# Optimization experiments

Measured on AMD Instinct MI355X. Metric: run time of the kernel, lower is better.

Reference implementation:

```python
import jax, jax.numpy as jnp
import numpy as np

H = 8
DH = 64  # attention_head_size
HID = 512
NEG = -90000000000.0

def _lin(x, w, b):
    return x @ w + b

def _tfs(x):  # [N, HID] -> [H, N, DH]
    n = x.shape[0]
    return x.reshape(n, H, DH).transpose(1, 0, 2)

def _cross(q, ck, v, cv, mask, dw, db):
    # q: [H,N,DH], ck/cv: [H,M,DH], v: [H,N,DH], mask: [N,M]
    s = jnp.einsum('hnd,hmd->hnm', q, ck)
    s = s * mask[None, :, :] / jnp.sqrt(jnp.asarray(DH, s.dtype))
    s = jnp.where(s == 0.0, NEG, s)  # faithful zero->-inf hack
    p = jax.nn.softmax(s, axis=-1)
    ctx = v + jnp.einsum('hnm,hmd->hnd', p, cv)  # residual add of raw value
    n = ctx.shape[1]
    ctx = ctx.transpose(1, 0, 2).reshape(n, H * DH)
    return _lin(ctx, dw, db)

def setup_inputs() -> dict:
    key = jax.random.key(0)
    ks = jax.random.split(key, 24)
    N1, N2, D1 = 4096, 4096, 300
    d = {}
    d['h_head'] = jax.random.normal(ks[0], (N1, D1), jnp.float32)
    d['h_tail'] = jax.random.normal(ks[1], (N2, HID), jnp.float32)
    d['batch_head'] = jnp.sort(jax.random.randint(ks[2], (N1,), 0, 64))
    d['batch_tail'] = jnp.sort(jax.random.randint(ks[3], (N2,), 0, 64))
    def w(k, i, o):
        return jax.random.normal(k, (i, o), jnp.float32) / np.sqrt(i)
    d['map_w'] = w(ks[4], D1, HID); d['map_b'] = jnp.zeros((HID,), jnp.float32)
    names = ['q1', 'k1', 'v1', 'q2', 'k2', 'v2', 'd1', 'd2']
    for i, nm in enumerate(names):
        d[nm + '_w'] = w(ks[5 + i], HID, HID)
        d[nm + '_b'] = jnp.zeros((HID,), jnp.float32)
    return d

def reference(h_head, h_tail, batch_head, batch_tail,
              map_w, map_b,
              q1_w, q1_b, k1_w, k1_b, v1_w, v1_b,
              q2_w, q2_b, k2_w, k2_b, v2_w, v2_b,
              d1_w, d1_b, d2_w, d2_b):
    hh = _lin(h_head, map_w, map_b)  # n_dim1 != n_dim2 -> map
    q_h = _tfs(_lin(hh, q1_w, q1_b))
    k_h = _tfs(_lin(hh, k1_w, k1_b))
    v_h = _tfs(_lin(hh, v1_w, v1_b))
    q_t = _tfs(_lin(h_tail, q2_w, q2_b))
    k_t = _tfs(_lin(h_tail, k2_w, k2_b))
    v_t = _tfs(_lin(h_tail, v2_w, v2_b))
    mask = (batch_head[:, None] == batch_tail[None, :]).astype(jnp.float32)
    out_head = _cross(q_h, k_t, v_h, v_t, mask, d1_w, d1_b)
    out_tail = _cross(q_t, k_h, v_t, v_h, mask.T, d2_w, d2_b)
    return (out_head, out_tail)
```

## Files before the change

### kernel.cpp

```cpp
#include <hip/hip_runtime.h>
#include <hip/hip_bf16.h>
#include <math.h>


typedef __bf16 bf16x8 __attribute__((ext_vector_type(8)));
typedef float  f32x4  __attribute__((ext_vector_type(4)));

#define HID 512
#define NTOK 4096

#define AS1(p) ((const __attribute__((address_space(1))) void*)(p))
#define AS3(p) ((__attribute__((address_space(3))) void*)(p))

__global__ __launch_bounds__(256) void prep_inputs(
    const float* __restrict__ h_head, const float* __restrict__ h_tail,
    const int* __restrict__ bh, const int* __restrict__ bt,
    __bf16* __restrict__ hh_bf, __bf16* __restrict__ ht_bf,
    int* __restrict__ ranges)
{
    const int q = blockIdx.x, z = blockIdx.z, tid = threadIdx.x;

    if (z == 0) {
        if (q == 0 && tid < 128) {
            int b = tid & 63;
            const int* arr = (tid < 64) ? bh : bt;
            int base = (tid < 64) ? 0 : 128;
            int lo = 0, hi = NTOK;
            while (lo < hi) { int mid = (lo + hi) >> 1; if (arr[mid] < b) lo = mid + 1; else hi = mid; }
            int start = lo;
            lo = 0; hi = NTOK;
            while (lo < hi) { int mid = (lo + hi) >> 1; if (arr[mid] <= b) lo = mid + 1; else hi = mid; }
            ranges[base + b] = start;
            ranges[base + 64 + b] = lo;
        }
        for (int idx = tid; idx < 8 * 40; idx += 256) {
            int r   = q * 8 + idx / 40;
            int col = (idx % 40) * 8;
            bf16x8 v;
            if (col + 8 <= 300) {
                float4 f0 = *(const float4*)&h_head[(size_t)r * 300 + col];
                float4 f1 = *(const float4*)&h_head[(size_t)r * 300 + col + 4];
                v[0]=(__bf16)f0.x; v[1]=(__bf16)f0.y; v[2]=(__bf16)f0.z; v[3]=(__bf16)f0.w;
                v[4]=(__bf16)f1.x; v[5]=(__bf16)f1.y; v[6]=(__bf16)f1.z; v[7]=(__bf16)f1.w;
            } else if (col < 300) {
                float4 f0 = *(const float4*)&h_head[(size_t)r * 300 + col];
                v[0]=(__bf16)f0.x; v[1]=(__bf16)f0.y; v[2]=(__bf16)f0.z; v[3]=(__bf16)f0.w;
                v[4]=(__bf16)0.f; v[5]=(__bf16)0.f; v[6]=(__bf16)0.f; v[7]=(__bf16)0.f;
            } else {
                #pragma unroll
                for (int j = 0; j < 8; ++j) v[j] = (__bf16)0.f;
            }
            *(bf16x8*)&hh_bf[(size_t)r * 320 + col] = v;
        }
    } else {
        for (int idx = tid; idx < 8 * 64; idx += 256) {
            int r   = q * 8 + (idx >> 6);
            int col = (idx & 63) * 8;
            float4 f0 = *(const float4*)&h_tail[(size_t)r * 512 + col];
            float4 f1 = *(const float4*)&h_tail[(size_t)r * 512 + col + 4];
            bf16x8 v;
            v[0]=(__bf16)f0.x; v[1]=(__bf16)f0.y; v[2]=(__bf16)f0.z; v[3]=(__bf16)f0.w;
            v[4]=(__bf16)f1.x; v[5]=(__bf16)f1.y; v[6]=(__bf16)f1.z; v[7]=(__bf16)f1.w;
            *(bf16x8*)&ht_bf[(size_t)r * 512 + col] = v;
        }
    }
}

struct TransJobs {
    const float* src[9];
    __bf16*      dst[9];
    int          K[9];
    int          ldT[9];
};

__global__ __launch_bounds__(256) void transpose_weights(TransJobs tj) {
    const int z = blockIdx.z;
    const float* src = tj.src[z];
    __bf16* dst = tj.dst[z];
    const int K = tj.K[z], ldT = tj.ldT[z];
    const int tk = blockIdx.y * 64;
    const int tn = blockIdx.x * 64;
    if (tk >= ldT) return;

    __shared__ __bf16 T[64][72];
    const int tid = threadIdx.x;
    const int r0 = tid >> 4;
    const int c0 = (tid & 15) * 4;
    #pragma unroll
    for (int i = 0; i < 4; ++i) {
        int k = tk + r0 + i * 16;
        float4 v = (k < K) ? *(const float4*)&src[(size_t)k * 512 + tn + c0]
                           : float4{0.f, 0.f, 0.f, 0.f};
        T[r0 + i * 16][c0 + 0] = (__bf16)v.x;
        T[r0 + i * 16][c0 + 1] = (__bf16)v.y;
        T[r0 + i * 16][c0 + 2] = (__bf16)v.z;
        T[r0 + i * 16][c0 + 3] = (__bf16)v.w;
    }
    __syncthreads();

    const int n  = tid >> 2;
    const int kk = (tid & 3) * 16;
    bf16x8 o0, o1;
    #pragma unroll
    for (int j = 0; j < 8; ++j) { o0[j] = T[kk + j][n]; o1[j] = T[kk + 8 + j][n]; }
    __bf16* dp = dst + (size_t)(tn + n) * ldT + tk + kk;
    *(bf16x8*)dp       = o0;
    *(bf16x8*)(dp + 8) = o1;
}

struct GemmJobs {
    const __bf16* A[4];
    const __bf16* W[4];
    const float*  bias[4];
    void*         C[4];
    int           Kp[4];
};

template <typename TC>
__global__ __launch_bounds__(256) void gemm128(GemmJobs jobs) {
    __shared__ __align__(16) __bf16 As[128 * 32];
    __shared__ __align__(16) __bf16 Bs[128 * 32];

    const int z = blockIdx.z;
    const __bf16* A    = jobs.A[z];
    const __bf16* W    = jobs.W[z];
    const float*  bias = jobs.bias[z];
    TC*           C    = (TC*)jobs.C[z];
    const int     Kp   = jobs.Kp[z];

    const int tid  = threadIdx.x;
    const int wave = tid >> 6;
    const int lane = tid & 63;
    const int quad = lane >> 4;
    const int l16  = lane & 15;
    const int wy   = wave >> 1;
    const int wx   = wave & 1;
    const int rowBase = blockIdx.y * 128;
    const int colBase = blockIdx.x * 128;

    const int s_row = tid >> 2;
    const int s_kc  = (tid & 3) * 8;

    f32x4 acc[4][4] = {};

    const __bf16* gA = A + (size_t)(rowBase + s_row) * Kp + s_kc;
    const __bf16* gB = W + (size_t)(colBase + s_row) * Kp + s_kc;
    __bf16* lA0 = &As[wave * 512];
    __bf16* lA1 = &As[2048 + wave * 512];
    __bf16* lB0 = &Bs[wave * 512];
    __bf16* lB1 = &Bs[2048 + wave * 512];

    for (int kt = 0; kt < Kp; kt += 32) {
        __builtin_amdgcn_global_load_lds(AS1(gA + kt),            AS3(lA0), 16, 0, 0);
        __builtin_amdgcn_global_load_lds(AS1(gA + kt + 64 * Kp),  AS3(lA1), 16, 0, 0);
        __builtin_amdgcn_global_load_lds(AS1(gB + kt),            AS3(lB0), 16, 0, 0);
        __builtin_amdgcn_global_load_lds(AS1(gB + kt + 64 * Kp),  AS3(lB1), 16, 0, 0);
        __syncthreads();

        bf16x8 ar[4], br[4];
        #pragma unroll
        for (int i = 0; i < 4; ++i)
            ar[i] = *(const bf16x8*)&As[(wy * 64 + i * 16 + l16) * 32 + quad * 8];
        #pragma unroll
        for (int j = 0; j < 4; ++j)
            br[j] = *(const bf16x8*)&Bs[(wx * 64 + j * 16 + l16) * 32 + quad * 8];
        #pragma unroll
        for (int i = 0; i < 4; ++i)
            #pragma unroll
            for (int j = 0; j < 4; ++j)
                acc[i][j] = __builtin_amdgcn_mfma_f32_16x16x32_bf16(ar[i], br[j], acc[i][j], 0, 0, 0);
        __syncthreads();
    }

    #pragma unroll
    for (int j = 0; j < 4; ++j) {
        int col = colBase + wx * 64 + j * 16 + l16;
        float bv = bias[col];
        #pragma unroll
        for (int i = 0; i < 4; ++i) {
            #pragma unroll
            for (int r = 0; r < 4; ++r) {
                int row = rowBase + wy * 64 + i * 16 + quad * 4 + r;
                C[(size_t)row * HID + col] = (TC)(acc[i][j][r] + bv);
            }
        }
    }
}

__global__ __launch_bounds__(256) void attn_mfma(
    const __bf16* __restrict__ Q0, const __bf16* __restrict__ K0,
    const __bf16* __restrict__ Vr0, const __bf16* __restrict__ Vc0,
    const __bf16* __restrict__ Q1, const __bf16* __restrict__ K1,
    const __bf16* __restrict__ Vr1, const __bf16* __restrict__ Vc1,
    const int* __restrict__ ranges,
    __bf16* __restrict__ O0, __bf16* __restrict__ O1,
    int Nq, int Nk)
{
    __shared__ __align__(16) __bf16 Qs[64][72];
    __shared__ __align__(16) __bf16 Ks[64][72];
    __shared__ __align__(16) __bf16 Vt[64][72];
    __shared__ __align__(16) __bf16 Ps[64][72];

    const int z = blockIdx.z;
    const __bf16* Q    = z ? Q1 : Q0;
    const __bf16* Kg   = z ? K1 : K0;
    const __bf16* Vres = z ? Vr1 : Vr0;
    const __bf16* Vctx = z ? Vc1 : Vc0;
    __bf16* Out        = z ? O1 : O0;
    const int* qstart  = z ? ranges + 128 : ranges;
    const int* qend    = z ? ranges + 192 : ranges + 64;
    const int* kstart  = z ? ranges       : ranges + 128;
    const int* kend    = z ? ranges + 64  : ranges + 192;

    const int h = blockIdx.x, b = blockIdx.y;
    const int qs = qstart[b], qe = qend[b];
    const int ts = kstart[b], te = kend[b];
    const int nq = qe - qs, nk = te - ts;
    if (nq <= 0) return;

    const int tid  = threadIdx.x;
    const int wave = tid >> 6;
    const int lane = tid & 63;
    const int quad = lane >> 4;
    const int l16  = lane & 15;
    const int srow = tid >> 2;
    const int scol = (tid & 3) * 16;

    if (nk <= 0) {
        float* meanv = (float*)Qs;
        if (tid < 64) {
            float s = 0.f;
            for (int m = 0; m < Nk; ++m)
                s += (float)Vctx[(size_t)m * HID + h * 64 + tid];
            meanv[tid] = s / (float)Nk;
        }
        __syncthreads();
        int d = tid & 63;
        for (int r = qs + (tid >> 6); r < qe; r += 4) {
            size_t off = (size_t)r * HID + h * 64 + d;
            Out[off] = (__bf16)((float)Vres[off] + meanv[d]);
        }
        return;
    }

    for (int qc = 0; qc < nq; qc += 64) {
        __syncthreads();
        {
            int qg = min(qs + qc + srow, Nq - 1);
            const __bf16* src = Q + (size_t)qg * HID + h * 64 + scol;
            *(bf16x8*)&Qs[srow][scol]     = *(const bf16x8*)src;
            *(bf16x8*)&Qs[srow][scol + 8] = *(const bf16x8*)(src + 8);
        }
        __syncthreads();
        bf16x8 aq0 = *(const bf16x8*)&Qs[wave * 16 + l16][quad * 8];
        bf16x8 aq1 = *(const bf16x8*)&Qs[wave * 16 + l16][32 + quad * 8];

        f32x4 O[4] = {};
        float Mx[4], L[4];
        #pragma unroll
        for (int r = 0; r < 4; ++r) { Mx[r] = -__builtin_inff(); L[r] = 0.f; }

        for (int kc = 0; kc < nk; kc += 64) {
            __syncthreads();
            {
                int kg = min(ts + kc + srow, Nk - 1);
                const __bf16* ksrc = Kg + (size_t)kg * HID + h * 64 + scol;
                *(bf16x8*)&Ks[srow][scol]     = *(const bf16x8*)ksrc;
                *(bf16x8*)&Ks[srow][scol + 8] = *(const bf16x8*)(ksrc + 8);
                const __bf16* vsrc = Vctx + (size_t)kg * HID + h * 64 + scol;
                bf16x8 v0 = *(const bf16x8*)vsrc;
                bf16x8 v1 = *(const bf16x8*)(vsrc + 8);
                #pragma unroll
                for (int j = 0; j < 8; ++j) {
                    Vt[scol + j][srow]     = v0[j];
                    Vt[scol + 8 + j][srow] = v1[j];
                }
            }
            __syncthreads();

            f32x4 S[4] = {};
            #pragma unroll
            for (int c = 0; c < 4; ++c) {
                bf16x8 bk0 = *(const bf16x8*)&Ks[c * 16 + l16][quad * 8];
                bf16x8 bk1 = *(const bf16x8*)&Ks[c * 16 + l16][32 + quad * 8];
                S[c] = __builtin_amdgcn_mfma_f32_16x16x32_bf16(aq0, bk0, S[c], 0, 0, 0);
                S[c] = __builtin_amdgcn_mfma_f32_16x16x32_bf16(aq1, bk1, S[c], 0, 0, 0);
            }

            #pragma unroll
            for (int c = 0; c < 4; ++c) {
                bool valid = (ts + kc + c * 16 + l16) < te;
                #pragma unroll
                for (int r = 0; r < 4; ++r)
                    S[c][r] = valid ? S[c][r] * 0.125f : -__builtin_inff();
            }

            float cm[4], ps[4], alpha[4];
            #pragma unroll
            for (int r = 0; r < 4; ++r) {
                float v = fmaxf(fmaxf(S[0][r], S[1][r]), fmaxf(S[2][r], S[3][r]));
                v = fmaxf(v, __shfl_xor(v, 1, 64));
                v = fmaxf(v, __shfl_xor(v, 2, 64));
                v = fmaxf(v, __shfl_xor(v, 4, 64));
                v = fmaxf(v, __shfl_xor(v, 8, 64));
                cm[r] = v;
            }
            #pragma unroll
            for (int r = 0; r < 4; ++r) {
                float nM = fmaxf(Mx[r], cm[r]);
                alpha[r] = __expf(Mx[r] - nM);
                Mx[r] = nM;
                ps[r] = 0.f;
            }
            #pragma unroll
            for (int c = 0; c < 4; ++c)
                #pragma unroll
                for (int r = 0; r < 4; ++r) {
                    float p = __expf(S[c][r] - Mx[r]);
                    S[c][r] = p;
                    ps[r] += p;
                }
            #pragma unroll
            for (int r = 0; r < 4; ++r) {
                float v = ps[r];
                v += __shfl_xor(v, 1, 64);
                v += __shfl_xor(v, 2, 64);
                v += __shfl_xor(v, 4, 64);
                v += __shfl_xor(v, 8, 64);
                L[r] = L[r] * alpha[r] + v;
            }
            #pragma unroll
            for (int c = 0; c < 4; ++c)
                #pragma unroll
                for (int r = 0; r < 4; ++r)
                    O[c][r] *= alpha[r];

            #pragma unroll
            for (int c = 0; c < 4; ++c)
                #pragma unroll
                for (int r = 0; r < 4; ++r)
                    Ps[wave * 16 + quad * 4 + r][c * 16 + l16] = (__bf16)S[c][r];
            __syncthreads();

            bf16x8 ap0 = *(const bf16x8*)&Ps[wave * 16 + l16][quad * 8];
            bf16x8 ap1 = *(const bf16x8*)&Ps[wave * 16 + l16][32 + quad * 8];
            #pragma unroll
            for (int c = 0; c < 4; ++c) {
                bf16x8 bv0 = *(const bf16x8*)&Vt[c * 16 + l16][quad * 8];
                bf16x8 bv1 = *(const bf16x8*)&Vt[c * 16 + l16][32 + quad * 8];
                O[c] = __builtin_amdgcn_mfma_f32_16x16x32_bf16(ap0, bv0, O[c], 0, 0, 0);
                O[c] = __builtin_amdgcn_mfma_f32_16x16x32_bf16(ap1, bv1, O[c], 0, 0, 0);
            }
        }

        #pragma unroll
        for (int c = 0; c < 4; ++c) {
            int d = h * 64 + c * 16 + l16;
            #pragma unroll
            for (int r = 0; r < 4; ++r) {
                int qrow = qs + qc + wave * 16 + quad * 4 + r;
                if (qrow < qe) {
                    size_t off = (size_t)qrow * HID + d;
                    Out[off] = (__bf16)((float)Vres[off] + O[c][r] / L[r]);
                }
            }
        }
    }
}

extern "C" void kernel_launch(void* const* d_in, const int* in_sizes, int n_in,
                              void* d_out, int out_size, void* d_ws, size_t ws_size,
                              hipStream_t stream) {
    (void)in_sizes; (void)n_in; (void)out_size; (void)ws_size;

    const float* h_head = (const float*)d_in[0];
    const float* h_tail = (const float*)d_in[1];
    const int* batch_head = (const int*)d_in[2];
    const int* batch_tail = (const int*)d_in[3];
    const float* map_w = (const float*)d_in[4];
    const float* map_b = (const float*)d_in[5];
    const float* q1_w = (const float*)d_in[6];
    const float* q1_b = (const float*)d_in[7];
    const float* k1_w = (const float*)d_in[8];
    const float* k1_b = (const float*)d_in[9];
    const float* v1_w = (const float*)d_in[10];
    const float* v1_b = (const float*)d_in[11];
    const float* q2_w = (const float*)d_in[12];
    const float* q2_b = (const float*)d_in[13];
    const float* k2_w = (const float*)d_in[14];
    const float* k2_b = (const float*)d_in[15];
    const float* v2_w = (const float*)d_in[16];
    const float* v2_b = (const float*)d_in[17];
    const float* d1_w = (const float*)d_in[18];
    const float* d1_b = (const float*)d_in[19];
    const float* d2_w = (const float*)d_in[20];
    const float* d2_b = (const float*)d_in[21];

    float* out = (float*)d_out;

    const size_t SZ = (size_t)NTOK * HID;
    char* ws = (char*)d_ws;
    int* ranges = (int*)ws;
    __bf16* hh   = (__bf16*)(ws + 1024);
    __bf16* qh   = hh  + SZ;
    __bf16* kh   = qh  + SZ;
    __bf16* vh   = kh  + SZ;
    __bf16* qt   = vh  + SZ;
    __bf16* kt   = qt  + SZ;
    __bf16* vt   = kt  + SZ;
    __bf16* ctxh = vt  + SZ;
    __bf16* ctxt = ctxh + SZ;
    __bf16* mapT = ctxt + SZ;
    __bf16* q1T  = mapT + 512 * 320;
    __bf16* k1T  = q1T + 512 * 512;
    __bf16* v1T  = k1T + 512 * 512;
    __bf16* q2T  = v1T + 512 * 512;
    __bf16* k2T  = q2T + 512 * 512;
    __bf16* v2T  = k2T + 512 * 512;
    __bf16* d1T  = v2T + 512 * 512;
    __bf16* d2T  = d1T + 512 * 512;
    __bf16* hh_bf = d2T + 512 * 512;
    __bf16* ht_bf = hh_bf + (size_t)NTOK * 320;

    prep_inputs<<<dim3(512, 1, 2), dim3(256), 0, stream>>>(
        h_head, h_tail, batch_head, batch_tail, hh_bf, ht_bf, ranges);

    TransJobs tj;
    tj.src[0] = map_w; tj.dst[0] = mapT; tj.K[0] = 300; tj.ldT[0] = 320;
    const float* wsrc[8] = {q1_w, k1_w, v1_w, q2_w, k2_w, v2_w, d1_w, d2_w};
    __bf16* wdst[8] = {q1T, k1T, v1T, q2T, k2T, v2T, d1T, d2T};
    for (int i = 0; i < 8; ++i) {
        tj.src[i + 1] = wsrc[i]; tj.dst[i + 1] = wdst[i];
        tj.K[i + 1] = 512; tj.ldT[i + 1] = 512;
    }
    transpose_weights<<<dim3(8, 8, 9), dim3(256), 0, stream>>>(tj);

    {
        GemmJobs j;
        j.A[0] = hh_bf; j.W[0] = mapT; j.bias[0] = map_b; j.C[0] = hh; j.Kp[0] = 320;
        j.A[1] = ht_bf; j.W[1] = q2T; j.bias[1] = q2_b; j.C[1] = qt; j.Kp[1] = 512;
        j.A[2] = ht_bf; j.W[2] = k2T; j.bias[2] = k2_b; j.C[2] = kt; j.Kp[2] = 512;
        j.A[3] = ht_bf; j.W[3] = v2T; j.bias[3] = v2_b; j.C[3] = vt; j.Kp[3] = 512;
        gemm128<__bf16><<<dim3(4, 32, 4), dim3(256), 0, stream>>>(j);
    }
    {
        GemmJobs j;
        j.A[0] = hh; j.W[0] = q1T; j.bias[0] = q1_b; j.C[0] = qh; j.Kp[0] = 512;
        j.A[1] = hh; j.W[1] = k1T; j.bias[1] = k1_b; j.C[1] = kh; j.Kp[1] = 512;
        j.A[2] = hh; j.W[2] = v1T; j.bias[2] = v1_b; j.C[2] = vh; j.Kp[2] = 512;
        j.A[3] = hh; j.W[3] = v1T; j.bias[3] = v1_b; j.C[3] = vh; j.Kp[3] = 512;
        gemm128<__bf16><<<dim3(4, 32, 3), dim3(256), 0, stream>>>(j);
    }

    attn_mfma<<<dim3(8, 64, 2), dim3(256), 0, stream>>>(
        qh, kt, vh, vt,
        qt, kh, vt, vh,
        ranges, ctxh, ctxt, NTOK, NTOK);

    {
        GemmJobs j;
        j.A[0] = ctxh; j.W[0] = d1T; j.bias[0] = d1_b; j.C[0] = out;      j.Kp[0] = 512;
        j.A[1] = ctxt; j.W[1] = d2T; j.bias[1] = d2_b; j.C[1] = out + SZ; j.Kp[1] = 512;
        j.A[2] = ctxt; j.W[2] = d2T; j.bias[2] = d2_b; j.C[2] = out + SZ; j.Kp[2] = 512;
        j.A[3] = ctxt; j.W[3] = d2T; j.bias[3] = d2_b; j.C[3] = out + SZ; j.Kp[3] = 512;
        gemm128<float><<<dim3(4, 32, 2), dim3(256), 0, stream>>>(j);
    }
}
```

Before: 191.7 us.

## Fold map projection into head QKV weights and software-pipeline GEMM loads

The map linear layer is folded algebraically into the q1/k1/v1 weights. A small GEMM computes map_w·W fused weights, and prep_inputs computes the fused biases map_b·W+b. This removes one serial 4096x512 GEMM launch and its intermediate buffer, and lets all six QKV projections run in a single launch. The GEMM also switches from direct global-to-LDS loads to register-prefetched double buffering with a launch-bounds occupancy hint. The fused weights are rounded to bf16 twice, which adds precision risk, and K is padded to 384.

Result: slower. 363.9 us (+89.9%).

```diff
diff --git a/kernel.cpp b/kernel.cpp
--- a/kernel.cpp
+++ b/kernel.cpp
@@ -8,14 +8,18 @@
 
 #define HID 512
 #define NTOK 4096
-
-#define AS1(p) ((const __attribute__((address_space(1))) void*)(p))
-#define AS3(p) ((__attribute__((address_space(3))) void*)(p))
+#define KHEAD 384
 
 __global__ __launch_bounds__(256) void prep_inputs(
     const float* __restrict__ h_head, const float* __restrict__ h_tail,
     const int* __restrict__ bh, const int* __restrict__ bt,
+    const float* __restrict__ map_w, const float* __restrict__ map_b,
+    const float* __restrict__ q1_w, const float* __restrict__ q1_b,
+    const float* __restrict__ k1_w, const float* __restrict__ k1_b,
+    const float* __restrict__ v1_w, const float* __restrict__ v1_b,
     __bf16* __restrict__ hh_bf, __bf16* __restrict__ ht_bf,
+    __bf16* __restrict__ map_bf,
+    float* __restrict__ fb, float* __restrict__ zbuf,
     int* __restrict__ ranges)
 {
     const int q = blockIdx.x, z = blockIdx.z, tid = threadIdx.x;
@@ -33,9 +37,9 @@
             ranges[base + b] = start;
             ranges[base + 64 + b] = lo;
         }
-        for (int idx = tid; idx < 8 * 40; idx += 256) {
-            int r   = q * 8 + idx / 40;
-            int col = (idx % 40) * 8;
+        for (int idx = tid; idx < 8 * 48; idx += 256) {
+            int r   = q * 8 + idx / 48;
+            int col = (idx % 48) * 8;
             bf16x8 v;
             if (col + 8 <= 300) {
                 float4 f0 = *(const float4*)&h_head[(size_t)r * 300 + col];
@@ -50,9 +54,9 @@
                 #pragma unroll
                 for (int j = 0; j < 8; ++j) v[j] = (__bf16)0.f;
             }
-            *(bf16x8*)&hh_bf[(size_t)r * 320 + col] = v;
-        }
-    } else {
+            *(bf16x8*)&hh_bf[(size_t)r * KHEAD + col] = v;
+        }
+    } else if (z == 1) {
         for (int idx = tid; idx < 8 * 64; idx += 256) {
             int r   = q * 8 + (idx >> 6);
             int col = (idx & 63) * 8;
@@ -63,24 +67,53 @@
             v[4]=(__bf16)f1.x; v[5]=(__bf16)f1.y; v[6]=(__bf16)f1.z; v[7]=(__bf16)f1.w;
             *(bf16x8*)&ht_bf[(size_t)r * 512 + col] = v;
         }
+    } else {
+        if (q < 96) {
+            int r = q * 4 + (tid >> 6);
+            int col = (tid & 63) * 8;
+            bf16x8 v;
+            if (r < 300) {
+                float4 f0 = *(const float4*)&map_w[(size_t)r * 512 + col];
+                float4 f1 = *(const float4*)&map_w[(size_t)r * 512 + col + 4];
+                v[0]=(__bf16)f0.x; v[1]=(__bf16)f0.y; v[2]=(__bf16)f0.z; v[3]=(__bf16)f0.w;
+                v[4]=(__bf16)f1.x; v[5]=(__bf16)f1.y; v[6]=(__bf16)f1.z; v[7]=(__bf16)f1.w;
+            } else {
+                #pragma unroll
+                for (int j = 0; j < 8; ++j) v[j] = (__bf16)0.f;
+            }
+            *(bf16x8*)&map_bf[(size_t)r * 512 + col] = v;
+        } else if (q < 102) {
+            __shared__ float sm[512];
+            sm[tid] = map_b[tid];
+            sm[tid + 256] = map_b[tid + 256];
+            __syncthreads();
+            int m = q - 96;
+            int x = m >> 1, half = m & 1;
+            int n = half * 256 + tid;
+            const float* xw = x == 0 ? q1_w : (x == 1 ? k1_w : v1_w);
+            const float* xb = x == 0 ? q1_b : (x == 1 ? k1_b : v1_b);
+            float s = xb[n];
+            for (int j = 0; j < 512; ++j)
+                s += sm[j] * xw[(size_t)j * 512 + n];
+            fb[x * 512 + n] = s;
+        } else if (q == 102) {
+            zbuf[tid] = 0.f;
+            zbuf[tid + 256] = 0.f;
+        }
     }
 }
 
-struct TransJobs {
-    const float* src[9];
-    __bf16*      dst[9];
-    int          K[9];
-    int          ldT[9];
+struct Trans8 {
+    const float* src[8];
+    __bf16*      dst[8];
 };
 
-__global__ __launch_bounds__(256) void transpose_weights(TransJobs tj) {
+__global__ __launch_bounds__(256) void transpose_weights(Trans8 tj) {
     const int z = blockIdx.z;
     const float* src = tj.src[z];
     __bf16* dst = tj.dst[z];
-    const int K = tj.K[z], ldT = tj.ldT[z];
     const int tk = blockIdx.y * 64;
     const int tn = blockIdx.x * 64;
-    if (tk >= ldT) return;
 
     __shared__ __bf16 T[64][72];
     const int tid = threadIdx.x;
@@ -89,8 +122,7 @@
     #pragma unroll
     for (int i = 0; i < 4; ++i) {
         int k = tk + r0 + i * 16;
-        float4 v = (k < K) ? *(const float4*)&src[(size_t)k * 512 + tn + c0]
-                           : float4{0.f, 0.f, 0.f, 0.f};
+        float4 v = *(const float4*)&src[(size_t)k * 512 + tn + c0];
         T[r0 + i * 16][c0 + 0] = (__bf16)v.x;
         T[r0 + i * 16][c0 + 1] = (__bf16)v.y;
         T[r0 + i * 16][c0 + 2] = (__bf16)v.z;
@@ -103,23 +135,24 @@
     bf16x8 o0, o1;
     #pragma unroll
     for (int j = 0; j < 8; ++j) { o0[j] = T[kk + j][n]; o1[j] = T[kk + 8 + j][n]; }
-    __bf16* dp = dst + (size_t)(tn + n) * ldT + tk + kk;
+    __bf16* dp = dst + (size_t)(tn + n) * 512 + tk + kk;
     *(bf16x8*)dp       = o0;
     *(bf16x8*)(dp + 8) = o1;
 }
 
 struct GemmJobs {
-    const __bf16* A[4];
-    const __bf16* W[4];
-    const float*  bias[4];
-    void*         C[4];
-    int           Kp[4];
+    const __bf16* A[6];
+    const __bf16* W[6];
+    const float*  bias[6];
+    void*         C[6];
+    int           Kp[6];
+    int           ldC[6];
 };
 
 template <typename TC>
-__global__ __launch_bounds__(256) void gemm128(GemmJobs jobs) {
-    __shared__ __align__(16) __bf16 As[128 * 32];
-    __shared__ __align__(16) __bf16 Bs[128 * 32];
+__global__ __launch_bounds__(256, 3) void gemm128(GemmJobs jobs) {
+    __shared__ __align__(16) __bf16 As[4096];
+    __shared__ __align__(16) __bf16 Bs[4096];
 
     const int z = blockIdx.z;
     const __bf16* A    = jobs.A[z];
@@ -127,6 +160,7 @@
     const float*  bias = jobs.bias[z];
     TC*           C    = (TC*)jobs.C[z];
     const int     Kp   = jobs.Kp[z];
+    const int     ldC  = jobs.ldC[z];
 
     const int tid  = threadIdx.x;
     const int wave = tid >> 6;
@@ -141,47 +175,63 @@
     const int s_row = tid >> 2;
     const int s_kc  = (tid & 3) * 8;
 
-    f32x4 acc[4][4] = {};
-
     const __bf16* gA = A + (size_t)(rowBase + s_row) * Kp + s_kc;
     const __bf16* gB = W + (size_t)(colBase + s_row) * Kp + s_kc;
-    __bf16* lA0 = &As[wave * 512];
-    __bf16* lA1 = &As[2048 + wave * 512];
-    __bf16* lB0 = &Bs[wave * 512];
-    __bf16* lB1 = &Bs[2048 + wave * 512];
-
-    for (int kt = 0; kt < Kp; kt += 32) {
-        __builtin_amdgcn_global_load_lds(AS1(gA + kt),            AS3(lA0), 16, 0, 0);
-        __builtin_amdgcn_global_load_lds(AS1(gA + kt + 64 * Kp),  AS3(lA1), 16, 0, 0);
-        __builtin_amdgcn_global_load_lds(AS1(gB + kt),            AS3(lB0), 16, 0, 0);
-        __builtin_amdgcn_global_load_lds(AS1(gB + kt + 64 * Kp),  AS3(lB1), 16, 0, 0);
+
+    f32x4 acc[4][4] = {};
+    bf16x8 pa0[2], pa1[2], pb0[2], pb1[2];
+    const int nk = Kp >> 5;
+
+    #pragma unroll
+    for (int s = 0; s < 2; ++s) {
+        int kt = s * 32;
+        pa0[s] = *(const bf16x8*)(gA + kt);
+        pa1[s] = *(const bf16x8*)(gA + kt + (size_t)64 * Kp);
+        pb0[s] = *(const bf16x8*)(gB + kt);
+        pb1[s] = *(const bf16x8*)(gB + kt + (size_t)64 * Kp);
+    }
+
+    for (int i = 0; i < nk; ++i) {
+        const int cur = i & 1;
+        if (i) __syncthreads();
+        *(bf16x8*)&As[tid * 8]        = pa0[cur];
+        *(bf16x8*)&As[2048 + tid * 8] = pa1[cur];
+        *(bf16x8*)&Bs[tid * 8]        = pb0[cur];
+        *(bf16x8*)&Bs[2048 + tid * 8] = pb1[cur];
         __syncthreads();
+
+        if (i + 2 < nk) {
+            int kt = (i + 2) * 32;
+            pa0[cur] = *(const bf16x8*)(gA + kt);
+            pa1[cur] = *(const bf16x8*)(gA + kt + (size_t)64 * Kp);
+            pb0[cur] = *(const bf16x8*)(gB + kt);
+            pb1[cur] = *(const bf16x8*)(gB + kt + (size_t)64 * Kp);
+        }
 
         bf16x8 ar[4], br[4];
         #pragma unroll
-        for (int i = 0; i < 4; ++i)
-            ar[i] = *(const bf16x8*)&As[(wy * 64 + i * 16 + l16) * 32 + quad * 8];
+        for (int ii = 0; ii < 4; ++ii)
+            ar[ii] = *(const bf16x8*)&As[(wy * 64 + ii * 16 + l16) * 32 + quad * 8];
         #pragma unroll
-        for (int j = 0; j < 4; ++j)
-            br[j] = *(const bf16x8*)&Bs[(wx * 64 + j * 16 + l16) * 32 + quad * 8];
+        for (int jj = 0; jj < 4; ++jj)
+            br[jj] = *(const bf16x8*)&Bs[(wx * 64 + jj * 16 + l16) * 32 + quad * 8];
         #pragma unroll
-        for (int i = 0; i < 4; ++i)
-            #pragma unroll
-            for (int j = 0; j < 4; ++j)
-                acc[i][j] = __builtin_amdgcn_mfma_f32_16x16x32_bf16(ar[i], br[j], acc[i][j], 0, 0, 0);
-        __syncthreads();
+        for (int ii = 0; ii < 4; ++ii)
+            #pragma unroll
+            for (int jj = 0; jj < 4; ++jj)
+                acc[ii][jj] = __builtin_amdgcn_mfma_f32_16x16x32_bf16(ar[ii], br[jj], acc[ii][jj], 0, 0, 0);
     }
 
     #pragma unroll
-    for (int j = 0; j < 4; ++j) {
-        int col = colBase + wx * 64 + j * 16 + l16;
+    for (int jj = 0; jj < 4; ++jj) {
+        int col = colBase + wx * 64 + jj * 16 + l16;
         float bv = bias[col];
         #pragma unroll
-        for (int i = 0; i < 4; ++i) {
+        for (int ii = 0; ii < 4; ++ii) {
             #pragma unroll
             for (int r = 0; r < 4; ++r) {
-                int row = rowBase + wy * 64 + i * 16 + quad * 4 + r;
-                C[(size_t)row * HID + col] = (TC)(acc[i][j][r] + bv);
+                int row = rowBase + wy * 64 + ii * 16 + quad * 4 + r;
+                C[(size_t)row * ldC + col] = (TC)(acc[ii][jj][r] + bv);
             }
         }
     }
@@ -401,8 +451,7 @@
     const size_t SZ = (size_t)NTOK * HID;
     char* ws = (char*)d_ws;
     int* ranges = (int*)ws;
-    __bf16* hh   = (__bf16*)(ws + 1024);
-    __bf16* qh   = hh  + SZ;
+    __bf16* qh   = (__bf16*)(ws + 1024);
     __bf16* kh   = qh  + SZ;
     __bf16* vh   = kh  + SZ;
     __bf16* qt   = vh  + SZ;
@@ -410,8 +459,7 @@
     __bf16* vt   = kt  + SZ;
     __bf16* ctxh = vt  + SZ;
     __bf16* ctxt = ctxh + SZ;
-    __bf16* mapT = ctxt + SZ;
-    __bf16* q1T  = mapT + 512 * 320;
+    __bf16* q1T  = ctxt + SZ;
     __bf16* k1T  = q1T + 512 * 512;
     __bf16* v1T  = k1T + 512 * 512;
     __bf16* q2T  = v1T + 512 * 512;
@@ -419,37 +467,43 @@
     __bf16* v2T  = k2T + 512 * 512;
     __bf16* d1T  = v2T + 512 * 512;
     __bf16* d2T  = d1T + 512 * 512;
-    __bf16* hh_bf = d2T + 512 * 512;
-    __bf16* ht_bf = hh_bf + (size_t)NTOK * 320;
-
-    prep_inputs<<<dim3(512, 1, 2), dim3(256), 0, stream>>>(
-        h_head, h_tail, batch_head, batch_tail, hh_bf, ht_bf, ranges);
-
-    TransJobs tj;
-    tj.src[0] = map_w; tj.dst[0] = mapT; tj.K[0] = 300; tj.ldT[0] = 320;
+    __bf16* hh_bf  = d2T + 512 * 512;
+    __bf16* ht_bf  = hh_bf + (size_t)NTOK * KHEAD;
+    __bf16* map_bf = ht_bf + SZ;
+    __bf16* fwqT   = map_bf + 384 * 512;
+    __bf16* fwkT   = fwqT + 512 * KHEAD;
+    __bf16* fwvT   = fwkT + 512 * KHEAD;
+    float*  fb     = (float*)(fwvT + 512 * KHEAD);
+    float*  zbuf   = fb + 3 * 512;
+
+    prep_inputs<<<dim3(512, 1, 3), dim3(256), 0, stream>>>(
+        h_head, h_tail, batch_head, batch_tail,
+        map_w, map_b, q1_w, q1_b, k1_w, k1_b, v1_w, v1_b,
+        hh_bf, ht_bf, map_bf, fb, zbuf, ranges);
+
+    Trans8 tj;
     const float* wsrc[8] = {q1_w, k1_w, v1_w, q2_w, k2_w, v2_w, d1_w, d2_w};
     __bf16* wdst[8] = {q1T, k1T, v1T, q2T, k2T, v2T, d1T, d2T};
-    for (int i = 0; i < 8; ++i) {
-        tj.src[i + 1] = wsrc[i]; tj.dst[i + 1] = wdst[i];
-        tj.K[i + 1] = 512; tj.ldT[i + 1] = 512;
-    }
-    transpose_weights<<<dim3(8, 8, 9), dim3(256), 0, stream>>>(tj);
+    for (int i = 0; i < 8; ++i) { tj.src[i] = wsrc[i]; tj.dst[i] = wdst[i]; }
+    transpose_weights<<<dim3(8, 8, 8), dim3(256), 0, stream>>>(tj);
 
     {
-        GemmJobs j;
-        j.A[0] = hh_bf; j.W[0] = mapT; j.bias[0] = map_b; j.C[0] = hh; j.Kp[0] = 320;
-        j.A[1] = ht_bf; j.W[1] = q2T; j.bias[1] = q2_b; j.C[1] = qt; j.Kp[1] = 512;
-        j.A[2] = ht_bf; j.W[2] = k2T; j.bias[2] = k2_b; j.C[2] = kt; j.Kp[2] = 512;
-        j.A[3] = ht_bf; j.W[3] = v2T; j.bias[3] = v2_b; j.C[3] = vt; j.Kp[3] = 512;
-        gemm128<__bf16><<<dim3(4, 32, 4), dim3(256), 0, stream>>>(j);
-    }
+        GemmJobs j = {};
+        j.A[0] = q1T; j.W[0] = map_bf; j.bias[0] = zbuf; j.C[0] = fwqT; j.Kp[0] = 512; j.ldC[0] = KHEAD;
+        j.A[1] = k1T; j.W[1] = map_bf; j.bias[1] = zbuf; j.C[1] = fwkT; j.Kp[1] = 512; j.ldC[1] = KHEAD;
+        j.A[2] = v1T; j.W[2] = map_bf; j.bias[2] = zbuf; j.C[2] = fwvT; j.Kp[2] = 512; j.ldC[2] = KHEAD;
+        gemm128<__bf16><<<dim3(3, 4, 3), dim3(256), 0, stream>>>(j);
+    }
+
     {
-        GemmJobs j;
-        j.A[0] = hh; j.W[0] = q1T; j.bias[0] = q1_b; j.C[0] = qh; j.Kp[0] = 512;
-        j.A[1] = hh; j.W[1] = k1T; j.bias[1] = k1_b; j.C[1] = kh; j.Kp[1] = 512;
-        j.A[2] = hh; j.W[2] = v1T; j.bias[2] = v1_b; j.C[2] = vh; j.Kp[2] = 512;
-        j.A[3] = hh; j.W[3] = v1T; j.bias[3] = v1_b; j.C[3] = vh; j.Kp[3] = 512;
-        gemm128<__bf16><<<dim3(4, 32, 3), dim3(256), 0, stream>>>(j);
+        GemmJobs j = {};
+        j.A[0] = hh_bf; j.W[0] = fwqT; j.bias[0] = fb;       j.C[0] = qh; j.Kp[0] = KHEAD; j.ldC[0] = 512;
+        j.A[1] = hh_bf; j.W[1] = fwkT; j.bias[1] = fb + 512; j.C[1] = kh; j.Kp[1] = KHEAD; j.ldC[1] = 512;
+        j.A[2] = hh_bf; j.W[2] = fwvT; j.bias[2] = fb + 1024;j.C[2] = vh; j.Kp[2] = KHEAD; j.ldC[2] = 512;
+        j.A[3] = ht_bf; j.W[3] = q2T;  j.bias[3] = q2_b;     j.C[3] = qt; j.Kp[3] = 512;   j.ldC[3] = 512;
+        j.A[4] = ht_bf; j.W[4] = k2T;  j.bias[4] = k2_b;     j.C[4] = kt; j.Kp[4] = 512;   j.ldC[4] = 512;
+        j.A[5] = ht_bf; j.W[5] = v2T;  j.bias[5] = v2_b;     j.C[5] = vt; j.Kp[5] = 512;   j.ldC[5] = 512;
+        gemm128<__bf16><<<dim3(4, 32, 6), dim3(256), 0, stream>>>(j);
     }
 
     attn_mfma<<<dim3(8, 64, 2), dim3(256), 0, stream>>>(
@@ -458,11 +512,9 @@
         ranges, ctxh, ctxt, NTOK, NTOK);
 
     {
-        GemmJobs j;
-        j.A[0] = ctxh; j.W[0] = d1T; j.bias[0] = d1_b; j.C[0] = out;      j.Kp[0] = 512;
-        j.A[1] = ctxt; j.W[1] = d2T; j.bias[1] = d2_b; j.C[1] = out + SZ; j.Kp[1] = 512;
-        j.A[2] = ctxt; j.W[2] = d2T; j.bias[2] = d2_b; j.C[2] = out + SZ; j.Kp[2] = 512;
-        j.A[3] = ctxt; j.W[3] = d2T; j.bias[3] = d2_b; j.C[3] = out + SZ; j.Kp[3] = 512;
+        GemmJobs j = {};
+        j.A[0] = ctxh; j.W[0] = d1T; j.bias[0] = d1_b; j.C[0] = out;      j.Kp[0] = 512; j.ldC[0] = 512;
+        j.A[1] = ctxt; j.W[1] = d2T; j.bias[1] = d2_b; j.C[1] = out + SZ; j.Kp[1] = 512; j.ldC[1] = 512;
         gemm128<float><<<dim3(4, 32, 2), dim3(256), 0, stream>>>(j);
     }
 }
```

## Double-buffer GEMM LDS tiles and XOR-swizzle k-chunks to avoid bank conflicts

Applied to the files above, without the earlier changes.

The projection GEMM now keeps two LDS buffers for A and B and issues the global-to-LDS loads for the next k-tile before computing the current one. This lets memory latency overlap with MFMA work and drops one barrier per iteration. It also XOR-swizzles the 8-element k-chunk position by row so the per-lane LDS reads spread across banks. LDS use doubles, which may lower occupancy, and correctness relies on the global source swizzle matching the read-side swizzle.

After: 186.7 us. -2.6%, faster.

```diff
diff --git a/kernel.cpp b/kernel.cpp
--- a/kernel.cpp
+++ b/kernel.cpp
@@ -118,8 +118,8 @@
 
 template <typename TC>
 __global__ __launch_bounds__(256) void gemm128(GemmJobs jobs) {
-    __shared__ __align__(16) __bf16 As[128 * 32];
-    __shared__ __align__(16) __bf16 Bs[128 * 32];
+    __shared__ __align__(16) __bf16 As[2][4096];
+    __shared__ __align__(16) __bf16 Bs[2][4096];
 
     const int z = blockIdx.z;
     const __bf16* A    = jobs.A[z];
@@ -139,49 +139,61 @@
     const int colBase = blockIdx.x * 128;
 
     const int s_row = tid >> 2;
-    const int s_kc  = (tid & 3) * 8;
-
-    f32x4 acc[4][4] = {};
+    const int s_kc  = ((tid & 3) ^ ((s_row >> 1) & 3)) * 8;
 
     const __bf16* gA = A + (size_t)(rowBase + s_row) * Kp + s_kc;
     const __bf16* gB = W + (size_t)(colBase + s_row) * Kp + s_kc;
-    __bf16* lA0 = &As[wave * 512];
-    __bf16* lA1 = &As[2048 + wave * 512];
-    __bf16* lB0 = &Bs[wave * 512];
-    __bf16* lB1 = &Bs[2048 + wave * 512];
-
-    for (int kt = 0; kt < Kp; kt += 32) {
-        __builtin_amdgcn_global_load_lds(AS1(gA + kt),            AS3(lA0), 16, 0, 0);
-        __builtin_amdgcn_global_load_lds(AS1(gA + kt + 64 * Kp),  AS3(lA1), 16, 0, 0);
-        __builtin_amdgcn_global_load_lds(AS1(gB + kt),            AS3(lB0), 16, 0, 0);
-        __builtin_amdgcn_global_load_lds(AS1(gB + kt + 64 * Kp),  AS3(lB1), 16, 0, 0);
+    const int waveOff = wave * 512;
+
+    f32x4 acc[4][4] = {};
+    const int nk = Kp >> 5;
+
+    __builtin_amdgcn_global_load_lds(AS1(gA),                   AS3(&As[0][waveOff]),        16, 0, 0);
+    __builtin_amdgcn_global_load_lds(AS1(gA + (size_t)64 * Kp), AS3(&As[0][2048 + waveOff]), 16, 0, 0);
+    __builtin_amdgcn_global_load_lds(AS1(gB),                   AS3(&Bs[0][waveOff]),        16, 0, 0);
+    __builtin_amdgcn_global_load_lds(AS1(gB + (size_t)64 * Kp), AS3(&Bs[0][2048 + waveOff]), 16, 0, 0);
+
+    for (int i = 0; i < nk; ++i) {
+        const int cur = i & 1;
         __syncthreads();
 
+        if (i + 1 < nk) {
+            const int kt = (i + 1) * 32;
+            const int nx = cur ^ 1;
+            __builtin_amdgcn_global_load_lds(AS1(gA + kt),                   AS3(&As[nx][waveOff]),        16, 0, 0);
+            __builtin_amdgcn_global_load_lds(AS1(gA + kt + (size_t)64 * Kp), AS3(&As[nx][2048 + waveOff]), 16, 0, 0);
+            __builtin_amdgcn_global_load_lds(AS1(gB + kt),                   AS3(&Bs[nx][waveOff]),        16, 0, 0);
+            __builtin_amdgcn_global_load_lds(AS1(gB + kt + (size_t)64 * Kp), AS3(&Bs[nx][2048 + waveOff]), 16, 0, 0);
+        }
+
         bf16x8 ar[4], br[4];
         #pragma unroll
-        for (int i = 0; i < 4; ++i)
-            ar[i] = *(const bf16x8*)&As[(wy * 64 + i * 16 + l16) * 32 + quad * 8];
-        #pragma unroll
-        for (int j = 0; j < 4; ++j)
-            br[j] = *(const bf16x8*)&Bs[(wx * 64 + j * 16 + l16) * 32 + quad * 8];
-        #pragma unroll
-        for (int i = 0; i < 4; ++i)
-            #pragma unroll
-            for (int j = 0; j < 4; ++j)
-                acc[i][j] = __builtin_amdgcn_mfma_f32_16x16x32_bf16(ar[i], br[j], acc[i][j], 0, 0, 0);
-        __syncthreads();
+        for (int ii = 0; ii < 4; ++ii) {
+            const int ra = wy * 64 + ii * 16 + l16;
+            ar[ii] = *(const bf16x8*)&As[cur][ra * 32 + ((quad ^ ((ra >> 1) & 3)) << 3)];
+        }
+        #pragma unroll
+        for (int jj = 0; jj < 4; ++jj) {
+            const int rb = wx * 64 + jj * 16 + l16;
+            br[jj] = *(const bf16x8*)&Bs[cur][rb * 32 + ((quad ^ ((rb >> 1) & 3)) << 3)];
+        }
+        #pragma unroll
+        for (int ii = 0; ii < 4; ++ii)
+            #pragma unroll
+            for (int jj = 0; jj < 4; ++jj)
+                acc[ii][jj] = __builtin_amdgcn_mfma_f32_16x16x32_bf16(ar[ii], br[jj], acc[ii][jj], 0, 0, 0);
     }
 
     #pragma unroll
-    for (int j = 0; j < 4; ++j) {
-        int col = colBase + wx * 64 + j * 16 + l16;
+    for (int jj = 0; jj < 4; ++jj) {
+        int col = colBase + wx * 64 + jj * 16 + l16;
         float bv = bias[col];
         #pragma unroll
-        for (int i = 0; i < 4; ++i) {
+        for (int ii = 0; ii < 4; ++ii) {
             #pragma unroll
             for (int r = 0; r < 4; ++r) {
-                int row = rowBase + wy * 64 + i * 16 + quad * 4 + r;
-                C[(size_t)row * HID + col] = (TC)(acc[i][j][r] + bv);
+                int row = rowBase + wy * 64 + ii * 16 + quad * 4 + r;
+                C[(size_t)row * HID + col] = (TC)(acc[ii][jj][r] + bv);
             }
         }
     }
```
